# Kernel optimization log

Hardware: AMD Instinct MI355X
Metric: run time of the kernel (lower is better)

Reference implementation:

```python
import jax, jax.numpy as jnp
import numpy as np

# Geometry constants (match init_kwargs)
PHI, T, H, W = 720, 512, 256, 256
ANGLE_RATIO = 1.0
RHO = float(np.sqrt(2.0))          # radius of detector span: ||max_pt-min_pt||/2 for [-1,1]^2
DPHI = float(np.pi) * ANGLE_RATIO / PHI   # uniform angle cell width (== mean angle step)
DT = 2.0 * RHO / T                 # detector cell width
T0 = -RHO + 0.5 * DT               # first detector cell center
DX = 2.0 / H                       # pixel width


def setup_inputs() -> dict:
    key = jax.random.key(0)
    k1, k2 = jax.random.split(key)
    sinos = jax.random.normal(k1, (32, PHI, T), dtype=jnp.float32)
    kernel = jax.random.normal(k2, (T // 2 + 1,), dtype=jnp.float32)
    return {"sinos": sinos, "kernel": kernel}


def _backproject(sino):
    """Parallel-beam backprojection (adjoint Radon), linear interp in t.

    sino: [B, PHI, T] -> image [B, H, W].
    f(x) = sum_phi g(phi, x.cos(phi)+y.sin(phi)) * dphi, zero outside detector.
    """
    angles = (jnp.arange(PHI, dtype=sino.dtype) + 0.5) * DPHI  # cell centers
    xs = (-1.0 + (jnp.arange(H, dtype=sino.dtype) + 0.5) * DX)
    X, Y = jnp.meshgrid(xs, xs, indexing='ij')  # [H, W] pixel centers

    def step(acc, inp):
        g, ang = inp                         # g: [B, T] sinogram slice at angle ang
        t = X * jnp.cos(ang) + Y * jnp.sin(ang)   # [H, W] detector coordinate
        u = (t - T0) / DT                    # fractional detector index
        i0 = jnp.floor(u)
        w = u - i0
        i0 = i0.astype(jnp.int32)
        i1 = i0 + 1
        w0 = jnp.where((i0 >= 0) & (i0 < T), 1.0 - w, 0.0)
        w1 = jnp.where((i1 >= 0) & (i1 < T), w, 0.0)
        i0c = jnp.clip(i0, 0, T - 1)
        i1c = jnp.clip(i1, 0, T - 1)
        v = g[:, i0c] * w0 + g[:, i1c] * w1  # [B, H, W]
        return acc + v, None

    B = sino.shape[0]
    acc0 = jnp.zeros((B, H, W), dtype=sino.dtype)
    sino_p = jnp.moveaxis(sino, 1, 0)        # [PHI, B, T] for scan over angles
    acc, _ = jax.lax.scan(step, acc0, (sino_p, angles))
    return acc * DPHI


def reference(sinos, kernel):
    # FFT-domain 1D filtering along detector axis, then backprojection
    filtered = jnp.fft.irfft(jnp.fft.rfft(sinos, axis=-1) * kernel, n=T, axis=-1)
    return _backproject(filtered.astype(sinos.dtype))
```

## Files before the change

### kernel.cpp

```cpp
#include <hip/hip_runtime.h>
#include <hip/hip_bf16.h>

#define NPHI 720
#define NT   512
#define NH   256
#define NB   32

#define DPHI_F   0.004363323129985824f
#define INV_DT_F 181.01933598375618f
#define DX_F     0.0078125f
#define W2PI_F   0.012271846303085130f

typedef __fp16  h2   __attribute__((ext_vector_type(2)));
typedef _Float16 f16x2 __attribute__((ext_vector_type(2)));
typedef _Float16 f16x8 __attribute__((ext_vector_type(8)));
typedef float    f32x4 __attribute__((ext_vector_type(4)));

__device__ __forceinline__ float fdot2f(h2 a, float b_bits, float c) {
    return __builtin_amdgcn_fdot2(__builtin_bit_cast(f16x2, a),
                                  __builtin_bit_cast(f16x2, b_bits), c, false);
}
__device__ __forceinline__ unsigned int f2h(float x) {
    h2 p = __builtin_amdgcn_cvt_pkrtz(x, x);
    return (unsigned int)__builtin_bit_cast(ushort2, p).x;
}

__global__ void build_tables_kernel(const float* __restrict__ kern,
                                    float* __restrict__ ws) {
    __shared__ float ctab[512];
    __shared__ float kk[257];
    const int t = threadIdx.x;
    if (t < 257) kk[t] = kern[t];
    ctab[t] = cosf((float)t * W2PI_F);
    __syncthreads();

    float acc = 0.f;
    for (int k = 1; k < 256; ++k)
        acc += kk[k] * ctab[(k * t) & 511];
    float h = (kk[0] + ((t & 1) ? -kk[256] : kk[256]) + 2.f * acc) * (1.f / 512.f);
    ws[t] = h;

    for (int p = t; p < NPHI; p += 512) {
        float ang = ((float)p + 0.5f) * DPHI_F;
        float s, c;
        sincosf(ang, &s, &c);
        float cd = c * INV_DT_F;
        float sd = s * INV_DT_F;
        ws[512 + 4 * p + 0] = cd;
        ws[512 + 4 * p + 1] = sd;
        ws[512 + 4 * p + 2] = cd * DX_F;
        ws[512 + 4 * p + 3] = sd * DX_F;
    }
}

__global__ __launch_bounds__(256) void ht_zero_kernel(const float* __restrict__ ws,
                                                      unsigned int* __restrict__ Ht,
                                                      float4* __restrict__ out4,
                                                      int nout4) {
    const int bid = (int)blockIdx.x;
    const int tid = threadIdx.x;
    if (bid < 64) {
        const int o  = bid * 8 + (tid >> 5);
        const int c0 = tid & 31;
        unsigned int* dst = Ht + (size_t)o * 256;
        #pragma unroll
        for (int k = 0; k < 8; ++k) {
            int mp = c0 + 32 * k;
            float lo = ws[(o - 2 * mp) & 511];
            float hi = ws[(o - 2 * mp - 1) & 511];
            h2 p = __builtin_amdgcn_cvt_pkrtz(lo, hi);
            dst[mp] = __builtin_bit_cast(unsigned int, p);
        }
    } else {
        const float4 z = make_float4(0.f, 0.f, 0.f, 0.f);
        for (int i = (bid - 64) * 256 + tid; i < nout4; i += 128 * 256)
            out4[i] = z;
    }
}

#define ASTR 40
#define BSTR 40

__global__ __launch_bounds__(256) void conv_gemm_kernel(const float* __restrict__ g,
                                                        const unsigned short* __restrict__ Ht,
                                                        float* __restrict__ filt) {
    __shared__ __attribute__((aligned(16))) unsigned short As[64 * ASTR];
    __shared__ __attribute__((aligned(16))) unsigned short Bs[256 * BSTR];
    const int tid = threadIdx.x;
    const int m0 = ((int)blockIdx.x >> 1) * 64;
    const int n0 = ((int)blockIdx.x & 1) * 256;

    const int w = tid >> 6, l = tid & 63;
    const int wm = (w >> 1) * 32, wn = (w & 1) * 128;
    const int fr = l & 15, g16 = l >> 4;

    const int arow = tid >> 2, aq = (tid & 3) * 8;

    f32x4 acc[2][8];
    #pragma unroll
    for (int i = 0; i < 2; ++i)
        #pragma unroll
        for (int j = 0; j < 8; ++j) acc[i][j] = (f32x4){0.f, 0.f, 0.f, 0.f};

    for (int k0 = 0; k0 < 512; k0 += 32) {
        __syncthreads();
        {
            const float* src = g + (size_t)(m0 + arow) * NT + (k0 + aq);
            float4 v0 = *(const float4*)src;
            float4 v1 = *(const float4*)(src + 4);
            h2 p0 = __builtin_amdgcn_cvt_pkrtz(v0.x, v0.y);
            h2 p1 = __builtin_amdgcn_cvt_pkrtz(v0.z, v0.w);
            h2 p2 = __builtin_amdgcn_cvt_pkrtz(v1.x, v1.y);
            h2 p3 = __builtin_amdgcn_cvt_pkrtz(v1.z, v1.w);
            *(float4*)&As[arow * ASTR + aq] =
                make_float4(__builtin_bit_cast(float, p0), __builtin_bit_cast(float, p1),
                            __builtin_bit_cast(float, p2), __builtin_bit_cast(float, p3));
        }
        {
            const float4* src = (const float4*)(Ht + (size_t)(n0 + tid) * NT + k0);
            float4 v0 = src[0], v1 = src[1], v2 = src[2], v3 = src[3];
            unsigned short* dst = &Bs[tid * BSTR];
            *(float4*)(dst)      = v0;
            *(float4*)(dst + 8)  = v1;
            *(float4*)(dst + 16) = v2;
            *(float4*)(dst + 24) = v3;
        }
        __syncthreads();

        f16x8 af[2], bf[8];
        #pragma unroll
        for (int i = 0; i < 2; ++i)
            af[i] = *(const f16x8*)&As[(wm + i * 16 + fr) * ASTR + g16 * 8];
        #pragma unroll
        for (int j = 0; j < 8; ++j)
            bf[j] = *(const f16x8*)&Bs[(wn + j * 16 + fr) * BSTR + g16 * 8];
        #pragma unroll
        for (int i = 0; i < 2; ++i)
            #pragma unroll
            for (int j = 0; j < 8; ++j)
                acc[i][j] = __builtin_amdgcn_mfma_f32_16x16x32_f16(af[i], bf[j], acc[i][j], 0, 0, 0);
    }

    #pragma unroll
    for (int i = 0; i < 2; ++i)
        #pragma unroll
        for (int j = 0; j < 8; ++j)
            #pragma unroll
            for (int v = 0; v < 4; ++v) {
                int row = m0 + wm + i * 16 + g16 * 4 + v;
                int col = n0 + wn + j * 16 + fr;
                filt[(size_t)row * NT + col] = acc[i][j][v];
            }
}

#define WCHUNK 15
#define WSTR   82

__global__ __launch_bounds__(256, 8) void backproject_kernel(const float* __restrict__ filt,
                                                             const float* __restrict__ ws,
                                                             float* __restrict__ out) {
    __shared__ __attribute__((aligned(16))) float4 win[WCHUNK][WSTR];
    __shared__ float cstbuf[WCHUNK];

    const int tid  = threadIdx.x;
    const int bidx = (int)blockIdx.x;
    const int quarter = bidx >> 9;
    const int rem  = bidx & 511;
    const int b    = (rem >> 6) * 4;
    const int tile = rem & 63;
    const int i0 = (tile >> 3) * 32;
    const int j0 = (tile & 7) * 32;

    const float* trig = ws + 512;

    const int w  = tid >> 6;
    const int l  = tid & 63;
    const int wi = (w >> 1) * 16, wj = (w & 1) * 16;
    const int li = l >> 3, lj = l & 7;
    const int pi = i0 + wi + 2 * li;
    const int pj = j0 + wj + 2 * lj;
    const float xi = -1.f + ((float)pi + 0.5f) * DX_F;
    const float yj = -1.f + ((float)pj + 0.5f) * DX_F;

    const int sa = tid >> 4;
    const int st = tid & 15;
    const float xlo = -1.f + ((float)i0 + 0.5f) * DX_F;
    const float xhi = xlo + 31.f * DX_F;
    const float ylo = -1.f + ((float)j0 + 0.5f) * DX_F;
    const float yhi = ylo + 31.f * DX_F;

    const float* fb0 = filt + (size_t)b * (NPHI * NT);

    float acc[4][2][2];
    #pragma unroll
    for (int bb = 0; bb < 4; ++bb)
        #pragma unroll
        for (int di = 0; di < 2; ++di)
            #pragma unroll
            for (int dj = 0; dj < 2; ++dj) acc[bb][di][dj] = 0.f;

    const int pbeg = quarter * 180;
    for (int p0 = pbeg; p0 < pbeg + 180; p0 += WCHUNK) {
        __syncthreads();
        if (sa < WCHUNK) {
            const int p = p0 + sa;
            const float4 tg = *(const float4*)&trig[p * 4];
            const float umin = 256.5f + fminf(xlo * tg.x, xhi * tg.x)
                                      + fminf(ylo * tg.y, yhi * tg.y);
            const float b0f = floorf(umin) - 1.f;
            if (st == 0) cstbuf[sa] = 256.5f - b0f;
            const int base = (int)b0f + 5 * st - 1;
            float f[4][6];
            #pragma unroll
            for (int bb = 0; bb < 4; ++bb) {
                const float* rr = fb0 + (size_t)bb * (NPHI * NT) + (size_t)p * NT;
                #pragma unroll
                for (int k = 0; k < 6; ++k) {
                    int idx = base + k;
                    f[bb][k] = ((unsigned)idx < 512u) ? rr[idx] : 0.f;
                }
            }
            float4* wr = &win[sa][5 * st];
            #pragma unroll
            for (int j = 0; j < 5; ++j) {
                h2 a0 = __builtin_amdgcn_cvt_pkrtz(f[0][j], f[0][j + 1]);
                h2 a1 = __builtin_amdgcn_cvt_pkrtz(f[1][j], f[1][j + 1]);
                h2 a2 = __builtin_amdgcn_cvt_pkrtz(f[2][j], f[2][j + 1]);
                h2 a3 = __builtin_amdgcn_cvt_pkrtz(f[3][j], f[3][j + 1]);
                wr[j] = make_float4(__builtin_bit_cast(float, a0),
                                    __builtin_bit_cast(float, a1),
                                    __builtin_bit_cast(float, a2),
                                    __builtin_bit_cast(float, a3));
            }
        }
        __syncthreads();

        #pragma unroll 3
        for (int a = 0; a < WCHUNK; ++a) {
            const float4 tg = *(const float4*)&trig[(p0 + a) * 4];
            const float cst = cstbuf[a];
            const float4* wr = &win[a][0];
            const float u00 = xi * tg.x + yj * tg.y + cst;
            #pragma unroll
            for (int di = 0; di < 2; ++di) {
                float u = di ? (u00 + tg.z) : u00;
                #pragma unroll
                for (int dj = 0; dj < 2; ++dj) {
                    float fl = floorf(u);
                    float wv = u - fl;
                    int  ip  = (int)fl;
                    h2   wp  = __builtin_amdgcn_cvt_pkrtz(1.f - wv, wv);
                    float4 s = wr[ip];
                    acc[0][di][dj] = fdot2f(wp, s.x, acc[0][di][dj]);
                    acc[1][di][dj] = fdot2f(wp, s.y, acc[1][di][dj]);
                    acc[2][di][dj] = fdot2f(wp, s.z, acc[2][di][dj]);
                    acc[3][di][dj] = fdot2f(wp, s.w, acc[3][di][dj]);
                    u += tg.w;
                }
            }
        }
    }

    #pragma unroll
    for (int bb = 0; bb < 4; ++bb) {
        float* ob = out + (size_t)(b + bb) * (NH * NH) + (size_t)pi * NH + pj;
        #pragma unroll
        for (int di = 0; di < 2; ++di)
            #pragma unroll
            for (int dj = 0; dj < 2; ++dj)
                unsafeAtomicAdd(ob + di * NH + dj, acc[bb][di][dj] * DPHI_F);
    }
}

extern "C" void kernel_launch(void* const* d_in, const int* in_sizes, int n_in,
                              void* d_out, int out_size, void* d_ws, size_t ws_size,
                              hipStream_t stream) {
    const float* sinos = (const float*)d_in[0];
    const float* kern  = (const float*)d_in[1];
    float* out = (float*)d_out;
    float* ws  = (float*)d_ws;

    unsigned int*   Ht32 = (unsigned int*)(ws + 4096);
    unsigned short* Ht   = (unsigned short*)Ht32;
    float*          filt = ws + 4096 + 131072;

    hipLaunchKernelGGL(build_tables_kernel, dim3(1), dim3(512), 0, stream, kern, ws);
    hipLaunchKernelGGL(ht_zero_kernel, dim3(192), dim3(256), 0, stream,
                       ws, Ht32, (float4*)out, out_size / 4);
    hipLaunchKernelGGL(conv_gemm_kernel, dim3((23040 / 64) * 2), dim3(256), 0, stream,
                       sinos, Ht, filt);
    hipLaunchKernelGGL(backproject_kernel, dim3(4 * (NB / 4) * 64), dim3(256), 0, stream,
                       filt, ws, out);
}
```

Before: 226.5 us.

## Merge setup kernels, pad filtered rows, retile GEMM to full-width N

Merges the table-building and Ht/zero kernels into one launch, with each Ht block recomputing the filter taps in shared memory. The filtered sinogram rows are padded to a stride of 520 with zeroed guard cells, so the backprojection window loads become unconditional vector loads instead of bounds-checked scalar loads. The conv GEMM now uses 32-row tiles covering all 512 columns, which removes the duplicate A loads across two N halves. The cost is 64 redundant filter-tap computations and more shared memory per GEMM block.

```diff
diff --git a/kernel.cpp b/kernel.cpp
--- a/kernel.cpp
+++ b/kernel.cpp
@@ -11,70 +11,79 @@
 #define DX_F     0.0078125f
 #define W2PI_F   0.012271846303085130f
 
+#define FSTR 520
+
 typedef __fp16  h2   __attribute__((ext_vector_type(2)));
 typedef _Float16 f16x2 __attribute__((ext_vector_type(2)));
 typedef _Float16 f16x8 __attribute__((ext_vector_type(8)));
 typedef float    f32x4 __attribute__((ext_vector_type(4)));
+typedef float    f32x4u __attribute__((ext_vector_type(4), aligned(4)));
+typedef float    f32x2u __attribute__((ext_vector_type(2), aligned(4)));
 
 __device__ __forceinline__ float fdot2f(h2 a, float b_bits, float c) {
     return __builtin_amdgcn_fdot2(__builtin_bit_cast(f16x2, a),
                                   __builtin_bit_cast(f16x2, b_bits), c, false);
 }
-__device__ __forceinline__ unsigned int f2h(float x) {
-    h2 p = __builtin_amdgcn_cvt_pkrtz(x, x);
-    return (unsigned int)__builtin_bit_cast(ushort2, p).x;
-}
-
-__global__ void build_tables_kernel(const float* __restrict__ kern,
-                                    float* __restrict__ ws) {
-    __shared__ float ctab[512];
-    __shared__ float kk[257];
-    const int t = threadIdx.x;
-    if (t < 257) kk[t] = kern[t];
-    ctab[t] = cosf((float)t * W2PI_F);
-    __syncthreads();
-
-    float acc = 0.f;
-    for (int k = 1; k < 256; ++k)
-        acc += kk[k] * ctab[(k * t) & 511];
-    float h = (kk[0] + ((t & 1) ? -kk[256] : kk[256]) + 2.f * acc) * (1.f / 512.f);
-    ws[t] = h;
-
-    for (int p = t; p < NPHI; p += 512) {
-        float ang = ((float)p + 0.5f) * DPHI_F;
-        float s, c;
-        sincosf(ang, &s, &c);
-        float cd = c * INV_DT_F;
-        float sd = s * INV_DT_F;
-        ws[512 + 4 * p + 0] = cd;
-        ws[512 + 4 * p + 1] = sd;
-        ws[512 + 4 * p + 2] = cd * DX_F;
-        ws[512 + 4 * p + 3] = sd * DX_F;
-    }
-}
-
-__global__ __launch_bounds__(256) void ht_zero_kernel(const float* __restrict__ ws,
-                                                      unsigned int* __restrict__ Ht,
-                                                      float4* __restrict__ out4,
-                                                      int nout4) {
+
+__global__ __launch_bounds__(256) void setup_kernel(const float* __restrict__ kern,
+                                                    float* __restrict__ ws,
+                                                    unsigned int* __restrict__ Ht,
+                                                    float4* __restrict__ out4,
+                                                    float* __restrict__ filt) {
     const int bid = (int)blockIdx.x;
     const int tid = threadIdx.x;
     if (bid < 64) {
+        __shared__ float ctab[512];
+        __shared__ float kk[257];
+        __shared__ float hloc[512];
+        kk[tid] = kern[tid];
+        if (tid == 0) kk[256] = kern[256];
+        ctab[tid]       = cosf((float)tid * W2PI_F);
+        ctab[tid + 256] = cosf((float)(tid + 256) * W2PI_F);
+        __syncthreads();
+        for (int tt = tid; tt < 512; tt += 256) {
+            float acc = 0.f;
+            for (int k = 1; k < 256; ++k)
+                acc += kk[k] * ctab[(k * tt) & 511];
+            hloc[tt] = (kk[0] + ((tt & 1) ? -kk[256] : kk[256]) + 2.f * acc) * (1.f / 512.f);
+        }
+        __syncthreads();
         const int o  = bid * 8 + (tid >> 5);
         const int c0 = tid & 31;
         unsigned int* dst = Ht + (size_t)o * 256;
         #pragma unroll
         for (int k = 0; k < 8; ++k) {
             int mp = c0 + 32 * k;
-            float lo = ws[(o - 2 * mp) & 511];
-            float hi = ws[(o - 2 * mp - 1) & 511];
-            h2 p = __builtin_amdgcn_cvt_pkrtz(lo, hi);
+            h2 p = __builtin_amdgcn_cvt_pkrtz(hloc[(o - 2 * mp) & 511],
+                                              hloc[(o - 2 * mp - 1) & 511]);
             dst[mp] = __builtin_bit_cast(unsigned int, p);
         }
+    } else if (bid < 67) {
+        int p = (bid - 64) * 256 + tid;
+        if (p < NPHI) {
+            float ang = ((float)p + 0.5f) * DPHI_F;
+            float s, c;
+            sincosf(ang, &s, &c);
+            float cd = c * INV_DT_F;
+            float sd = s * INV_DT_F;
+            ws[512 + 4 * p + 0] = cd;
+            ws[512 + 4 * p + 1] = sd;
+            ws[512 + 4 * p + 2] = cd * DX_F;
+            ws[512 + 4 * p + 3] = sd * DX_F;
+        }
+    } else if (bid < 195) {
+        const float4 z = make_float4(0.f, 0.f, 0.f, 0.f);
+        const int nout4 = NB * NH * NH / 4;
+        for (int i = (bid - 67) * 256 + tid; i < nout4; i += 128 * 256)
+            out4[i] = z;
     } else {
         const float4 z = make_float4(0.f, 0.f, 0.f, 0.f);
-        for (int i = (bid - 64) * 256 + tid; i < nout4; i += 128 * 256)
-            out4[i] = z;
+        const int rb = (bid - 195) * 180;
+        for (int i = tid; i < 360; i += 256) {
+            int row = rb + (i >> 1);
+            float* p = filt + (size_t)row * FSTR + ((i & 1) ? 516 : 0);
+            *(float4*)p = z;
+        }
     }
 }
 
@@ -84,17 +93,16 @@
 __global__ __launch_bounds__(256) void conv_gemm_kernel(const float* __restrict__ g,
                                                         const unsigned short* __restrict__ Ht,
                                                         float* __restrict__ filt) {
-    __shared__ __attribute__((aligned(16))) unsigned short As[64 * ASTR];
-    __shared__ __attribute__((aligned(16))) unsigned short Bs[256 * BSTR];
+    __shared__ __attribute__((aligned(16))) unsigned short As[32 * ASTR];
+    __shared__ __attribute__((aligned(16))) unsigned short Bs[512 * BSTR];
     const int tid = threadIdx.x;
-    const int m0 = ((int)blockIdx.x >> 1) * 64;
-    const int n0 = ((int)blockIdx.x & 1) * 256;
+    const int m0 = (int)blockIdx.x * 32;
 
     const int w = tid >> 6, l = tid & 63;
-    const int wm = (w >> 1) * 32, wn = (w & 1) * 128;
+    const int wn = w * 128;
     const int fr = l & 15, g16 = l >> 4;
 
-    const int arow = tid >> 2, aq = (tid & 3) * 8;
+    const int arow = tid >> 3, aq = (tid & 7) * 4;
 
     f32x4 acc[2][8];
     #pragma unroll
@@ -106,31 +114,32 @@
         __syncthreads();
         {
             const float* src = g + (size_t)(m0 + arow) * NT + (k0 + aq);
-            float4 v0 = *(const float4*)src;
-            float4 v1 = *(const float4*)(src + 4);
-            h2 p0 = __builtin_amdgcn_cvt_pkrtz(v0.x, v0.y);
-            h2 p1 = __builtin_amdgcn_cvt_pkrtz(v0.z, v0.w);
-            h2 p2 = __builtin_amdgcn_cvt_pkrtz(v1.x, v1.y);
-            h2 p3 = __builtin_amdgcn_cvt_pkrtz(v1.z, v1.w);
-            *(float4*)&As[arow * ASTR + aq] =
-                make_float4(__builtin_bit_cast(float, p0), __builtin_bit_cast(float, p1),
-                            __builtin_bit_cast(float, p2), __builtin_bit_cast(float, p3));
+            float4 v = *(const float4*)src;
+            h2 p0 = __builtin_amdgcn_cvt_pkrtz(v.x, v.y);
+            h2 p1 = __builtin_amdgcn_cvt_pkrtz(v.z, v.w);
+            *(uint2*)&As[arow * ASTR + aq] =
+                make_uint2(__builtin_bit_cast(unsigned int, p0),
+                           __builtin_bit_cast(unsigned int, p1));
         }
         {
-            const float4* src = (const float4*)(Ht + (size_t)(n0 + tid) * NT + k0);
-            float4 v0 = src[0], v1 = src[1], v2 = src[2], v3 = src[3];
-            unsigned short* dst = &Bs[tid * BSTR];
-            *(float4*)(dst)      = v0;
-            *(float4*)(dst + 8)  = v1;
-            *(float4*)(dst + 16) = v2;
-            *(float4*)(dst + 24) = v3;
+            #pragma unroll
+            for (int rr = 0; rr < 2; ++rr) {
+                const int row = tid + 256 * rr;
+                const float4* src = (const float4*)(Ht + (size_t)row * NT + k0);
+                float4 v0 = src[0], v1 = src[1], v2 = src[2], v3 = src[3];
+                unsigned short* dst = &Bs[row * BSTR];
+                *(float4*)(dst)      = v0;
+                *(float4*)(dst + 8)  = v1;
+                *(float4*)(dst + 16) = v2;
+                *(float4*)(dst + 24) = v3;
+            }
         }
         __syncthreads();
 
         f16x8 af[2], bf[8];
         #pragma unroll
         for (int i = 0; i < 2; ++i)
-            af[i] = *(const f16x8*)&As[(wm + i * 16 + fr) * ASTR + g16 * 8];
+            af[i] = *(const f16x8*)&As[(i * 16 + fr) * ASTR + g16 * 8];
         #pragma unroll
         for (int j = 0; j < 8; ++j)
             bf[j] = *(const f16x8*)&Bs[(wn + j * 16 + fr) * BSTR + g16 * 8];
@@ -147,9 +156,9 @@
         for (int j = 0; j < 8; ++j)
             #pragma unroll
             for (int v = 0; v < 4; ++v) {
-                int row = m0 + wm + i * 16 + g16 * 4 + v;
-                int col = n0 + wn + j * 16 + fr;
-                filt[(size_t)row * NT + col] = acc[i][j][v];
+                int row = m0 + i * 16 + g16 * 4 + v;
+                int col = wn + j * 16 + fr;
+                filt[(size_t)row * FSTR + 4 + col] = acc[i][j][v];
             }
 }
 
@@ -189,7 +198,7 @@
     const float ylo = -1.f + ((float)j0 + 0.5f) * DX_F;
     const float yhi = ylo + 31.f * DX_F;
 
-    const float* fb0 = filt + (size_t)b * (NPHI * NT);
+    const float* fb0 = filt + (size_t)b * (NPHI * FSTR);
 
     float acc[4][2][2];
     #pragma unroll
@@ -202,25 +211,26 @@
     const int pbeg = quarter * 180;
     for (int p0 = pbeg; p0 < pbeg + 180; p0 += WCHUNK) {
         __syncthreads();
-        if (sa < WCHUNK) {
+        if (sa < WCHUNK && st < 14) {
             const int p = p0 + sa;
             const float4 tg = *(const float4*)&trig[p * 4];
             const float umin = 256.5f + fminf(xlo * tg.x, xhi * tg.x)
                                       + fminf(ylo * tg.y, yhi * tg.y);
             const float b0f = floorf(umin) - 1.f;
             if (st == 0) cstbuf[sa] = 256.5f - b0f;
-            const int base = (int)b0f + 5 * st - 1;
+            const int b0 = (int)b0f;
+            const int base  = b0 + 5 * st - 1;
+            const int basec = min(base, 506);
             float f[4][6];
             #pragma unroll
             for (int bb = 0; bb < 4; ++bb) {
-                const float* rr = fb0 + (size_t)bb * (NPHI * NT) + (size_t)p * NT;
-                #pragma unroll
-                for (int k = 0; k < 6; ++k) {
-                    int idx = base + k;
-                    f[bb][k] = ((unsigned)idx < 512u) ? rr[idx] : 0.f;
-                }
-            }
-            float4* wr = &win[sa][5 * st];
+                const float* rr = fb0 + (size_t)bb * (NPHI * FSTR) + (size_t)p * FSTR + 4 + basec;
+                f32x4u v0 = *(const f32x4u*)rr;
+                f32x2u v1 = *(const f32x2u*)(rr + 4);
+                f[bb][0] = v0[0]; f[bb][1] = v0[1]; f[bb][2] = v0[2];
+                f[bb][3] = v0[3]; f[bb][4] = v1[0]; f[bb][5] = v1[1];
+            }
+            float4* wr = &win[sa][basec - b0 + 1];
             #pragma unroll
             for (int j = 0; j < 5; ++j) {
                 h2 a0 = __builtin_amdgcn_cvt_pkrtz(f[0][j], f[0][j + 1]);
@@ -284,10 +294,9 @@
     unsigned short* Ht   = (unsigned short*)Ht32;
     float*          filt = ws + 4096 + 131072;
 
-    hipLaunchKernelGGL(build_tables_kernel, dim3(1), dim3(512), 0, stream, kern, ws);
-    hipLaunchKernelGGL(ht_zero_kernel, dim3(192), dim3(256), 0, stream,
-                       ws, Ht32, (float4*)out, out_size / 4);
-    hipLaunchKernelGGL(conv_gemm_kernel, dim3((23040 / 64) * 2), dim3(256), 0, stream,
+    hipLaunchKernelGGL(setup_kernel, dim3(323), dim3(256), 0, stream,
+                       kern, ws, Ht32, (float4*)out, filt);
+    hipLaunchKernelGGL(conv_gemm_kernel, dim3(23040 / 32), dim3(256), 0, stream,
                        sinos, Ht, filt);
     hipLaunchKernelGGL(backproject_kernel, dim3(4 * (NB / 4) * 64), dim3(256), 0, stream,
                        filt, ws, out);
```

Result: no change. 225.6 us (-0.4%).
